# Optimization experiments

Measured on AMD Instinct MI355X. Metric: run time of the kernel, lower is better.

## Reference

```python
import jax, jax.numpy as jnp
import numpy as np

N_ATOMS = 500_000
N_BONDS = 600_000
N_MOL = 25_000
DEG_COUNTS = [100_000, 175_000, 150_000, 75_000]  # degrees 1..4, sum = N_ATOMS
ATOM_F, BOND_F = 62, 6
HID, FP = 100, 512


def setup_inputs() -> dict:
    key = jax.random.key(0)
    ks = jax.random.split(key, 32)
    inp = {}
    inp['atom_features'] = jax.random.normal(ks[0], (N_ATOMS, ATOM_F), dtype=jnp.float32)
    inp['bond_features'] = jax.random.normal(ks[1], (N_BONDS, BOND_F), dtype=jnp.float32)
    for i, (name_a, name_b, n) in enumerate(zip(['an1','an2','an3','an4'], ['bn1','bn2','bn3','bn4'], DEG_COUNTS)):
        d = i + 1
        inp[name_a] = jax.random.randint(ks[2 + 2*i], (n, d), 0, N_ATOMS, dtype=jnp.int32)
        inp[name_b] = jax.random.randint(ks[3 + 2*i], (n, d), 0, N_BONDS, dtype=jnp.int32)
    inp['mol_ids'] = jnp.repeat(jnp.arange(N_MOL, dtype=jnp.int32), N_ATOMS // N_MOL)
    dims = [(ATOM_F, HID), (HID, HID), (HID, FP)]
    for li, (din, dout) in enumerate(dims):
        inp[f'Wself{li}'] = jax.random.normal(ks[12 + li], (din, dout), dtype=jnp.float32) * (din ** -0.5)
        inp[f'bself{li}'] = jax.random.normal(ks[15 + li], (dout,), dtype=jnp.float32) * 0.01
        inp[f'Wd{li}'] = jax.random.normal(ks[18 + li], (4, din + BOND_F, dout), dtype=jnp.float32) * ((din + BOND_F) ** -0.5)
        inp[f'bd{li}'] = jax.random.normal(ks[21 + li], (4, dout), dtype=jnp.float32) * 0.01
    return inp


def _forward(atom_features, bond_features, ans, bns, mol_ids, self_params, deg_params):
    x = atom_features
    for (Ws, bs), (Wd, bd) in zip(self_params, deg_params):
        self_logits = x @ Ws + bs                      # [N, out]
        neigh = []
        for d in range(4):                             # degrees 1..4 (structurally distinct)
            a_sum = x[ans[d]].sum(axis=1)              # [n_d, F_in]  gather + reduce over degree
            b_sum = bond_features[bns[d]].sum(axis=1)  # [n_d, BOND_F]
            h = jnp.concatenate([a_sum, b_sum], axis=1)
            neigh.append(h @ Wd[d] + bd[d])
        neighbors_logits = jnp.concatenate(neigh, axis=0)  # atoms sorted by degree
        t = neighbors_logits + self_logits
        norm = jnp.linalg.norm(t, axis=1, keepdims=True)   # F.normalize (L2, eps=1e-12)
        x = jax.nn.relu(t / jnp.maximum(norm, 1e-12))
    return jax.ops.segment_sum(x, mol_ids, num_segments=N_MOL)  # sum_and_stack


def reference(atom_features, bond_features, an1, an2, an3, an4, bn1, bn2, bn3, bn4,
              mol_ids, Wself0, bself0, Wself1, bself1, Wself2, bself2,
              Wd0, bd0, Wd1, bd1, Wd2, bd2):
    ans = (an1, an2, an3, an4)
    bns = (bn1, bn2, bn3, bn4)
    self_params = ((Wself0, bself0), (Wself1, bself1), (Wself2, bself2))
    deg_params = ((Wd0, bd0), (Wd1, bd1), (Wd2, bd2))
    return _forward(atom_features, bond_features, ans, bns, mol_ids, self_params, deg_params)
```

## Files before the change

### kernel.cpp

```cpp
#include <hip/hip_runtime.h>


#define XS 100

typedef __attribute__((ext_vector_type(8))) short short8;
typedef __attribute__((ext_vector_type(4))) float float4v;

__device__ __forceinline__ float bf2f(unsigned u) { return __uint_as_float(u << 16); }
__device__ __forceinline__ unsigned short f2bf(float f) {
    unsigned b = __float_as_uint(f);
    return (unsigned short)((b + 0x7FFFu + ((b >> 16) & 1u)) >> 16);
}
__device__ __forceinline__ unsigned pack2(float a, float b) {
    return (unsigned)f2bf(a) | ((unsigned)f2bf(b) << 16);
}

__global__ void prep_weights(const float* __restrict__ Ws, const float* __restrict__ bs,
                             const float* __restrict__ Wd, const float* __restrict__ bd,
                             int F_IN, int F_OUT, int F_OUT_PAD, int KP, int SELF_PAD,
                             unsigned short* __restrict__ Wt, float* __restrict__ bc)
{
    int id = blockIdx.x * 256 + threadIdx.x;
    int total = 4 * F_OUT_PAD * KP;
    if (id >= total) return;
    int k  = id % KP;
    int nq = (id / KP) % F_OUT_PAD;
    int dg = id / (KP * F_OUT_PAD);
    float v = 0.f;
    if (nq < F_OUT) {
        if (k < F_IN)                                   v = Ws[(size_t)k * F_OUT + nq];
        else if (k >= SELF_PAD && k < SELF_PAD + F_IN)  v = Wd[((size_t)dg * (F_IN + 6) + (k - SELF_PAD)) * F_OUT + nq];
        else if (k >= 2 * SELF_PAD && k < 2 * SELF_PAD + 6)
            v = Wd[((size_t)dg * (F_IN + 6) + F_IN + (k - 2 * SELF_PAD)) * F_OUT + nq];
    }
    Wt[id] = f2bf(v);
    if (k == 0)
        bc[dg * F_OUT_PAD + nq] = (nq < F_OUT) ? (bs[nq] + bd[(size_t)dg * F_OUT + nq]) : 0.f;
}

template<int DEG, int SP>
__device__ __forceinline__ void gather_bf16(
    unsigned short* Hs, const unsigned short* __restrict__ x,
    const float* __restrict__ bondf,
    const int* __restrict__ an, const int* __restrict__ bn,
    int seg, int B40)
{
    const int tid = threadIdx.x;
    const int ch  = tid & 31;
    const int rr  = tid >> 5;

    if (ch < 25) {
        int ai[5][DEG];
        #pragma unroll
        for (int p = 0; p < 5; ++p) {
            const int ri = B40 + rr + 8 * p;
            #pragma unroll
            for (int d = 0; d < DEG; ++d) ai[p][d] = an[(size_t)ri * DEG + d];
        }
        uint2 sv[5], nv[5][DEG];
        #pragma unroll
        for (int p = 0; p < 5; ++p) {
            const int atom = seg + B40 + rr + 8 * p;
            sv[p] = *(const uint2*)(x + (size_t)atom * XS + ch * 4);
            #pragma unroll
            for (int d = 0; d < DEG; ++d)
                nv[p][d] = *(const uint2*)(x + (size_t)ai[p][d] * XS + ch * 4);
        }
        #pragma unroll
        for (int p = 0; p < 5; ++p) {
            unsigned short* hrow = Hs + (rr + 8 * p) * SP;
            *(uint2*)(hrow + ch * 4) = sv[p];
            float s0 = 0.f, s1 = 0.f, s2 = 0.f, s3 = 0.f;
            #pragma unroll
            for (int d = 0; d < DEG; ++d) {
                s0 += bf2f(nv[p][d].x & 0xFFFFu); s1 += bf2f(nv[p][d].x >> 16);
                s2 += bf2f(nv[p][d].y & 0xFFFFu); s3 += bf2f(nv[p][d].y >> 16);
            }
            uint2 o; o.x = pack2(s0, s1); o.y = pack2(s2, s3);
            *(uint2*)(hrow + 104 + ch * 4) = o;
        }
    }
    if (tid < 40) {
        const int ri = B40 + tid;
        int bi[DEG];
        #pragma unroll
        for (int d = 0; d < DEG; ++d) bi[d] = bn[(size_t)ri * DEG + d];
        float2 v0[DEG], v1[DEG], v2[DEG];
        #pragma unroll
        for (int d = 0; d < DEG; ++d) {
            const float* bp = bondf + (size_t)bi[d] * 6;
            v0[d] = *(const float2*)bp;
            v1[d] = *(const float2*)(bp + 2);
            v2[d] = *(const float2*)(bp + 4);
        }
        float s0 = 0.f, s1 = 0.f, s2 = 0.f, s3 = 0.f, s4 = 0.f, s5 = 0.f;
        #pragma unroll
        for (int d = 0; d < DEG; ++d) {
            s0 += v0[d].x; s1 += v0[d].y; s2 += v1[d].x;
            s3 += v1[d].y; s4 += v2[d].x; s5 += v2[d].y;
        }
        unsigned short* hrow = Hs + tid * SP;
        uint4 w; w.x = pack2(s0, s1); w.y = pack2(s2, s3); w.z = pack2(s4, s5); w.w = 0;
        *(uint4*)(hrow + 208) = w;
        *(uint4*)(hrow + 216) = make_uint4(0, 0, 0, 0);
    }
    for (int i = tid; i < 80; i += 256) {
        unsigned short* p = Hs + (i >> 1) * SP + ((i & 1) ? 204 : 100);
        *(uint2*)p = make_uint2(0, 0);
    }
    for (int i = tid; i < 8 * 28; i += 256) {
        *(uint4*)(Hs + (40 + i / 28) * SP + (i % 28) * 8) = make_uint4(0, 0, 0, 0);
    }
}

template<int DEG, int SP>
__device__ __forceinline__ void gather_f32(
    unsigned short* Hs, const float* __restrict__ x,
    const float* __restrict__ bondf,
    const int* __restrict__ an, const int* __restrict__ bn,
    int seg, int B40)
{
    const int tid = threadIdx.x;
    const int ch  = tid & 31;
    const int rr  = tid >> 5;

    if (ch < 31) {
        int ai[5][DEG];
        #pragma unroll
        for (int p = 0; p < 5; ++p) {
            const int ri = B40 + rr + 8 * p;
            #pragma unroll
            for (int d = 0; d < DEG; ++d) ai[p][d] = an[(size_t)ri * DEG + d];
        }
        float2 sv[5], nv[5][DEG];
        #pragma unroll
        for (int p = 0; p < 5; ++p) {
            const int atom = seg + B40 + rr + 8 * p;
            sv[p] = *(const float2*)(x + (size_t)atom * 62 + ch * 2);
            #pragma unroll
            for (int d = 0; d < DEG; ++d)
                nv[p][d] = *(const float2*)(x + (size_t)ai[p][d] * 62 + ch * 2);
        }
        #pragma unroll
        for (int p = 0; p < 5; ++p) {
            unsigned short* hrow = Hs + (rr + 8 * p) * SP;
            *(unsigned*)(hrow + ch * 2) = pack2(sv[p].x, sv[p].y);
            float s0 = 0.f, s1 = 0.f;
            #pragma unroll
            for (int d = 0; d < DEG; ++d) { s0 += nv[p][d].x; s1 += nv[p][d].y; }
            *(unsigned*)(hrow + 64 + ch * 2) = pack2(s0, s1);
        }
    }
    if (tid < 40) {
        const int ri = B40 + tid;
        int bi[DEG];
        #pragma unroll
        for (int d = 0; d < DEG; ++d) bi[d] = bn[(size_t)ri * DEG + d];
        float2 v0[DEG], v1[DEG], v2[DEG];
        #pragma unroll
        for (int d = 0; d < DEG; ++d) {
            const float* bp = bondf + (size_t)bi[d] * 6;
            v0[d] = *(const float2*)bp;
            v1[d] = *(const float2*)(bp + 2);
            v2[d] = *(const float2*)(bp + 4);
        }
        float s0 = 0.f, s1 = 0.f, s2 = 0.f, s3 = 0.f, s4 = 0.f, s5 = 0.f;
        #pragma unroll
        for (int d = 0; d < DEG; ++d) {
            s0 += v0[d].x; s1 += v0[d].y; s2 += v1[d].x;
            s3 += v1[d].y; s4 += v2[d].x; s5 += v2[d].y;
        }
        unsigned short* hrow = Hs + tid * SP;
        uint4 w; w.x = pack2(s0, s1); w.y = pack2(s2, s3); w.z = pack2(s4, s5); w.w = 0;
        *(uint4*)(hrow + 128) = w;
        *(uint4*)(hrow + 136) = make_uint4(0, 0, 0, 0);
        *(uint4*)(hrow + 144) = make_uint4(0, 0, 0, 0);
        *(uint4*)(hrow + 152) = make_uint4(0, 0, 0, 0);
    }
    for (int i = tid; i < 80; i += 256) {
        *(unsigned*)(Hs + (i >> 1) * SP + ((i & 1) ? 126 : 62)) = 0;
    }
    for (int i = tid; i < 8 * 20; i += 256) {
        *(uint4*)(Hs + (40 + i / 20) * SP + (i % 20) * 8) = make_uint4(0, 0, 0, 0);
    }
}

template<int F_IN, int F_OUT, int F_OUT_PAD, int SELF_PAD, bool LAST, bool BF16IN>
__global__ __launch_bounds__(256) void layer_mfma(
    const void* __restrict__ xin,
    const float* __restrict__ bondf,
    const int* __restrict__ an1, const int* __restrict__ bn1,
    const int* __restrict__ an2, const int* __restrict__ bn2,
    const int* __restrict__ an3, const int* __restrict__ bn3,
    const int* __restrict__ an4, const int* __restrict__ bn4,
    const unsigned short* __restrict__ Wt,
    const float* __restrict__ bcomb,
    unsigned short* __restrict__ xout,
    float* __restrict__ molout)
{
    constexpr int KP   = (2 * SELF_PAD + 6 + 31) & ~31;
    constexpr int SP   = KP + 8;
    constexpr int NT   = F_OUT_PAD / 16;
    constexpr int JMAX = (NT + 3) / 4;

    __shared__ __align__(16) unsigned short Hs[48 * SP];
    __shared__ float ssqs[4][48];

    const int R0 = blockIdx.x * 40;
    int deg, seg;
    if (R0 < 100000)      { deg = 1; seg = 0;      }
    else if (R0 < 275000) { deg = 2; seg = 100000; }
    else if (R0 < 425000) { deg = 3; seg = 275000; }
    else                  { deg = 4; seg = 425000; }
    const int B40 = R0 - seg;

    if constexpr (BF16IN) {
        const unsigned short* x = (const unsigned short*)xin;
        switch (deg) {
            case 1: gather_bf16<1, SP>(Hs, x, bondf, an1, bn1, seg, B40); break;
            case 2: gather_bf16<2, SP>(Hs, x, bondf, an2, bn2, seg, B40); break;
            case 3: gather_bf16<3, SP>(Hs, x, bondf, an3, bn3, seg, B40); break;
            default: gather_bf16<4, SP>(Hs, x, bondf, an4, bn4, seg, B40); break;
        }
    } else {
        const float* x = (const float*)xin;
        switch (deg) {
            case 1: gather_f32<1, SP>(Hs, x, bondf, an1, bn1, seg, B40); break;
            case 2: gather_f32<2, SP>(Hs, x, bondf, an2, bn2, seg, B40); break;
            case 3: gather_f32<3, SP>(Hs, x, bondf, an3, bn3, seg, B40); break;
            default: gather_f32<4, SP>(Hs, x, bondf, an4, bn4, seg, B40); break;
        }
    }
    __syncthreads();

    const int lane = threadIdx.x & 63;
    const int wv   = threadIdx.x >> 6;
    const int n16  = lane & 15;
    const int quad = lane >> 4;

    float4v acc[JMAX][3];
    #pragma unroll
    for (int j = 0; j < JMAX; ++j)
        #pragma unroll
        for (int mt = 0; mt < 3; ++mt)
            acc[j][mt] = (float4v){0.f, 0.f, 0.f, 0.f};

    const unsigned short* Wb = Wt + (size_t)(deg - 1) * F_OUT_PAD * KP;

    for (int kk = 0; kk < KP; kk += 32) {
        short8 a[3];
        #pragma unroll
        for (int mt = 0; mt < 3; ++mt)
            a[mt] = *(const short8*)&Hs[(mt * 16 + n16) * SP + kk + quad * 8];
        short8 b[JMAX];
        #pragma unroll
        for (int j = 0; j < JMAX; ++j) {
            const int nt = wv + 4 * j;
            if (nt < NT)
                b[j] = *(const short8*)(Wb + (size_t)(nt * 16 + n16) * KP + kk + quad * 8);
        }
        #pragma unroll
        for (int j = 0; j < JMAX; ++j) {
            const int nt = wv + 4 * j;
            if (nt < NT)
                #pragma unroll
                for (int mt = 0; mt < 3; ++mt)
                    acc[j][mt] = __builtin_amdgcn_mfma_f32_16x16x32_bf16(
                        a[mt], b[j], acc[j][mt], 0, 0, 0);
        }
    }

    float ssq[3][4];
    #pragma unroll
    for (int mt = 0; mt < 3; ++mt)
        #pragma unroll
        for (int r = 0; r < 4; ++r) ssq[mt][r] = 0.f;

    #pragma unroll
    for (int j = 0; j < JMAX; ++j) {
        const int nt = wv + 4 * j;
        if (nt < NT) {
            const float bj = bcomb[(deg - 1) * F_OUT_PAD + nt * 16 + n16];
            #pragma unroll
            for (int mt = 0; mt < 3; ++mt)
                #pragma unroll
                for (int r = 0; r < 4; ++r) {
                    float t = acc[j][mt][r] + bj;
                    acc[j][mt][r] = t;
                    ssq[mt][r] += t * t;
                }
        }
    }
    #pragma unroll
    for (int off = 1; off <= 8; off <<= 1)
        #pragma unroll
        for (int mt = 0; mt < 3; ++mt)
            #pragma unroll
            for (int r = 0; r < 4; ++r)
                ssq[mt][r] += __shfl_xor(ssq[mt][r], off);
    if (n16 == 0)
        #pragma unroll
        for (int mt = 0; mt < 3; ++mt)
            #pragma unroll
            for (int r = 0; r < 4; ++r)
                ssqs[wv][mt * 16 + quad * 4 + r] = ssq[mt][r];
    __syncthreads();

    float rn[3][4];
    #pragma unroll
    for (int mt = 0; mt < 3; ++mt)
        #pragma unroll
        for (int r = 0; r < 4; ++r) {
            const int row = mt * 16 + quad * 4 + r;
            const float s = ssqs[0][row] + ssqs[1][row] + ssqs[2][row] + ssqs[3][row];
            rn[mt][r] = 1.0f / fmaxf(sqrtf(s), 1e-12f);
        }

    if constexpr (!LAST) {
        #pragma unroll
        for (int j = 0; j < JMAX; ++j) {
            const int nt = wv + 4 * j;
            if (nt < NT) {
                const int col = nt * 16 + n16;
                if (col < F_OUT) {
                    #pragma unroll
                    for (int mt = 0; mt < 3; ++mt)
                        #pragma unroll
                        for (int r = 0; r < 4; ++r) {
                            const int row = mt * 16 + quad * 4 + r;
                            if (row < 40) {
                                const float v = fmaxf(acc[j][mt][r] * rn[mt][r], 0.f);
                                xout[(size_t)(R0 + row) * XS + col] = f2bf(v);
                            }
                        }
                }
            }
        }
    } else {
        #pragma unroll
        for (int j = 0; j < JMAX; ++j) {
            float m0 = 0.f, m1 = 0.f;
            #pragma unroll
            for (int mt = 0; mt < 3; ++mt)
                #pragma unroll
                for (int r = 0; r < 4; ++r) {
                    const int row = mt * 16 + quad * 4 + r;
                    if (row < 40) {
                        const float v = fmaxf(acc[j][mt][r] * rn[mt][r], 0.f);
                        if (row < 20) m0 += v; else m1 += v;
                    }
                }
            m0 += __shfl_xor(m0, 16); m0 += __shfl_xor(m0, 32);
            m1 += __shfl_xor(m1, 16); m1 += __shfl_xor(m1, 32);
            if (quad == 0) {
                const int col = (wv + 4 * j) * 16 + n16;
                molout[(size_t)(2 * blockIdx.x)     * 512 + col] = m0;
                molout[(size_t)(2 * blockIdx.x + 1) * 512 + col] = m1;
            }
        }
    }
}

extern "C" void kernel_launch(void* const* d_in, const int* in_sizes, int n_in,
                              void* d_out, int out_size, void* d_ws, size_t ws_size,
                              hipStream_t stream) {
    const bool sig_order = (in_sizes[3] != 100000);

    const float* atomf = (const float*)d_in[0];
    const float* bondf = (const float*)d_in[1];
    const int *an1, *bn1, *an2, *bn2, *an3, *bn3, *an4, *bn4;
    const float *Ws0, *bs0, *Wd0, *bd0;
    const float *Ws1, *bs1, *Wd1, *bd1;
    const float *Ws2, *bs2, *Wd2, *bd2;

    if (!sig_order) {
        an1 = (const int*)d_in[2];  bn1 = (const int*)d_in[3];
        an2 = (const int*)d_in[4];  bn2 = (const int*)d_in[5];
        an3 = (const int*)d_in[6];  bn3 = (const int*)d_in[7];
        an4 = (const int*)d_in[8];  bn4 = (const int*)d_in[9];
        Ws0 = (const float*)d_in[11]; bs0 = (const float*)d_in[12];
        Wd0 = (const float*)d_in[13]; bd0 = (const float*)d_in[14];
        Ws1 = (const float*)d_in[15]; bs1 = (const float*)d_in[16];
        Wd1 = (const float*)d_in[17]; bd1 = (const float*)d_in[18];
        Ws2 = (const float*)d_in[19]; bs2 = (const float*)d_in[20];
        Wd2 = (const float*)d_in[21]; bd2 = (const float*)d_in[22];
    } else {
        an1 = (const int*)d_in[2];  an2 = (const int*)d_in[3];
        an3 = (const int*)d_in[4];  an4 = (const int*)d_in[5];
        bn1 = (const int*)d_in[6];  bn2 = (const int*)d_in[7];
        bn3 = (const int*)d_in[8];  bn4 = (const int*)d_in[9];
        Ws0 = (const float*)d_in[11]; bs0 = (const float*)d_in[12];
        Ws1 = (const float*)d_in[13]; bs1 = (const float*)d_in[14];
        Ws2 = (const float*)d_in[15]; bs2 = (const float*)d_in[16];
        Wd0 = (const float*)d_in[17]; bd0 = (const float*)d_in[18];
        Wd1 = (const float*)d_in[19]; bd1 = (const float*)d_in[20];
        Wd2 = (const float*)d_in[21]; bd2 = (const float*)d_in[22];
    }

    char* w = (char*)d_ws;
    unsigned short* x1  = (unsigned short*)w;
    unsigned short* x2  = (unsigned short*)(w + 100000000);
    unsigned short* Wt0 = (unsigned short*)(w + 200000000);
    float*          bc0 = (float*)(w + 200143360);
    unsigned short* Wt1 = (unsigned short*)(w + 200145152);
    float*          bc1 = (float*)(w + 200345856);
    unsigned short* Wt2 = (unsigned short*)(w + 200347648);
    float*          bc2 = (float*)(w + 201265152);

    prep_weights<<<(4 * 112 * 160 + 255) / 256, 256, 0, stream>>>(
        Ws0, bs0, Wd0, bd0, 62, 100, 112, 160, 64, Wt0, bc0);
    prep_weights<<<(4 * 112 * 224 + 255) / 256, 256, 0, stream>>>(
        Ws1, bs1, Wd1, bd1, 100, 100, 112, 224, 104, Wt1, bc1);
    prep_weights<<<(4 * 512 * 224 + 255) / 256, 256, 0, stream>>>(
        Ws2, bs2, Wd2, bd2, 100, 512, 512, 224, 104, Wt2, bc2);

    dim3 grid(12500), block(256);
    layer_mfma<62, 100, 112, 64, false, false><<<grid, block, 0, stream>>>(
        atomf, bondf, an1, bn1, an2, bn2, an3, bn3, an4, bn4,
        Wt0, bc0, x1, nullptr);
    layer_mfma<100, 100, 112, 104, false, true><<<grid, block, 0, stream>>>(
        x1, bondf, an1, bn1, an2, bn2, an3, bn3, an4, bn4,
        Wt1, bc1, x2, nullptr);
    layer_mfma<100, 512, 512, 104, true, true><<<grid, block, 0, stream>>>(
        x2, bondf, an1, bn1, an2, bn2, an3, bn3, an4, bn4,
        Wt2, bc2, nullptr, (float*)d_out);
}
```

Before: 899.5 us.

## Double block size to 512 threads and spread gather and MFMA work over eight waves

```diff
diff --git a/kernel.cpp b/kernel.cpp
--- a/kernel.cpp
+++ b/kernel.cpp
@@ -47,70 +47,79 @@
 {
     const int tid = threadIdx.x;
     const int ch  = tid & 31;
-    const int rr  = tid >> 5;
+    const int rg  = tid >> 5;
 
     if (ch < 25) {
-        int ai[5][DEG];
-        #pragma unroll
-        for (int p = 0; p < 5; ++p) {
-            const int ri = B40 + rr + 8 * p;
-            #pragma unroll
-            for (int d = 0; d < DEG; ++d) ai[p][d] = an[(size_t)ri * DEG + d];
-        }
-        uint2 sv[5], nv[5][DEG];
-        #pragma unroll
-        for (int p = 0; p < 5; ++p) {
-            const int atom = seg + B40 + rr + 8 * p;
-            sv[p] = *(const uint2*)(x + (size_t)atom * XS + ch * 4);
-            #pragma unroll
-            for (int d = 0; d < DEG; ++d)
-                nv[p][d] = *(const uint2*)(x + (size_t)ai[p][d] * XS + ch * 4);
-        }
-        #pragma unroll
-        for (int p = 0; p < 5; ++p) {
-            unsigned short* hrow = Hs + (rr + 8 * p) * SP;
-            *(uint2*)(hrow + ch * 4) = sv[p];
-            float s0 = 0.f, s1 = 0.f, s2 = 0.f, s3 = 0.f;
+        int ai[3][DEG];
+        #pragma unroll
+        for (int p = 0; p < 3; ++p) {
+            const int r = rg + 16 * p;
+            if (r < 40) {
+                const int ri = B40 + r;
+                #pragma unroll
+                for (int d = 0; d < DEG; ++d) ai[p][d] = an[(size_t)ri * DEG + d];
+            }
+        }
+        uint2 sv[3], nv[3][DEG];
+        #pragma unroll
+        for (int p = 0; p < 3; ++p) {
+            const int r = rg + 16 * p;
+            if (r < 40) {
+                sv[p] = *(const uint2*)(x + (size_t)(seg + B40 + r) * XS + ch * 4);
+                #pragma unroll
+                for (int d = 0; d < DEG; ++d)
+                    nv[p][d] = *(const uint2*)(x + (size_t)ai[p][d] * XS + ch * 4);
+            }
+        }
+        #pragma unroll
+        for (int p = 0; p < 3; ++p) {
+            const int r = rg + 16 * p;
+            if (r < 40) {
+                unsigned short* hrow = Hs + r * SP;
+                *(uint2*)(hrow + ch * 4) = sv[p];
+                float s0 = 0.f, s1 = 0.f, s2 = 0.f, s3 = 0.f;
+                #pragma unroll
+                for (int d = 0; d < DEG; ++d) {
+                    s0 += bf2f(nv[p][d].x & 0xFFFFu); s1 += bf2f(nv[p][d].x >> 16);
+                    s2 += bf2f(nv[p][d].y & 0xFFFFu); s3 += bf2f(nv[p][d].y >> 16);
+                }
+                uint2 o; o.x = pack2(s0, s1); o.y = pack2(s2, s3);
+                *(uint2*)(hrow + 104 + ch * 4) = o;
+            }
+        }
+    } else {
+        const int idx = rg * 7 + (ch - 25);
+        if (idx < 40) {
+            const int ri = B40 + idx;
+            int bi[DEG];
+            #pragma unroll
+            for (int d = 0; d < DEG; ++d) bi[d] = bn[(size_t)ri * DEG + d];
+            float2 v0[DEG], v1[DEG], v2[DEG];
             #pragma unroll
             for (int d = 0; d < DEG; ++d) {
-                s0 += bf2f(nv[p][d].x & 0xFFFFu); s1 += bf2f(nv[p][d].x >> 16);
-                s2 += bf2f(nv[p][d].y & 0xFFFFu); s3 += bf2f(nv[p][d].y >> 16);
-            }
-            uint2 o; o.x = pack2(s0, s1); o.y = pack2(s2, s3);
-            *(uint2*)(hrow + 104 + ch * 4) = o;
-        }
-    }
-    if (tid < 40) {
-        const int ri = B40 + tid;
-        int bi[DEG];
-        #pragma unroll
-        for (int d = 0; d < DEG; ++d) bi[d] = bn[(size_t)ri * DEG + d];
-        float2 v0[DEG], v1[DEG], v2[DEG];
-        #pragma unroll
-        for (int d = 0; d < DEG; ++d) {
-            const float* bp = bondf + (size_t)bi[d] * 6;
-            v0[d] = *(const float2*)bp;
-            v1[d] = *(const float2*)(bp + 2);
-            v2[d] = *(const float2*)(bp + 4);
-        }
-        float s0 = 0.f, s1 = 0.f, s2 = 0.f, s3 = 0.f, s4 = 0.f, s5 = 0.f;
-        #pragma unroll
-        for (int d = 0; d < DEG; ++d) {
-            s0 += v0[d].x; s1 += v0[d].y; s2 += v1[d].x;
-            s3 += v1[d].y; s4 += v2[d].x; s5 += v2[d].y;
-        }
-        unsigned short* hrow = Hs + tid * SP;
-        uint4 w; w.x = pack2(s0, s1); w.y = pack2(s2, s3); w.z = pack2(s4, s5); w.w = 0;
-        *(uint4*)(hrow + 208) = w;
-        *(uint4*)(hrow + 216) = make_uint4(0, 0, 0, 0);
-    }
-    for (int i = tid; i < 80; i += 256) {
+                const float* bp = bondf + (size_t)bi[d] * 6;
+                v0[d] = *(const float2*)bp;
+                v1[d] = *(const float2*)(bp + 2);
+                v2[d] = *(const float2*)(bp + 4);
+            }
+            float s0 = 0.f, s1 = 0.f, s2 = 0.f, s3 = 0.f, s4 = 0.f, s5 = 0.f;
+            #pragma unroll
+            for (int d = 0; d < DEG; ++d) {
+                s0 += v0[d].x; s1 += v0[d].y; s2 += v1[d].x;
+                s3 += v1[d].y; s4 += v2[d].x; s5 += v2[d].y;
+            }
+            unsigned short* hrow = Hs + idx * SP;
+            uint4 w; w.x = pack2(s0, s1); w.y = pack2(s2, s3); w.z = pack2(s4, s5); w.w = 0;
+            *(uint4*)(hrow + 208) = w;
+            *(uint4*)(hrow + 216) = make_uint4(0, 0, 0, 0);
+        }
+    }
+    for (int i = tid; i < 80; i += 512) {
         unsigned short* p = Hs + (i >> 1) * SP + ((i & 1) ? 204 : 100);
         *(uint2*)p = make_uint2(0, 0);
     }
-    for (int i = tid; i < 8 * 28; i += 256) {
+    for (int i = tid; i < 8 * 28; i += 512)
         *(uint4*)(Hs + (40 + i / 28) * SP + (i % 28) * 8) = make_uint4(0, 0, 0, 0);
-    }
 }
 
 template<int DEG, int SP>
@@ -122,33 +131,41 @@
 {
     const int tid = threadIdx.x;
     const int ch  = tid & 31;
-    const int rr  = tid >> 5;
+    const int rg  = tid >> 5;
 
     if (ch < 31) {
-        int ai[5][DEG];
-        #pragma unroll
-        for (int p = 0; p < 5; ++p) {
-            const int ri = B40 + rr + 8 * p;
-            #pragma unroll
-            for (int d = 0; d < DEG; ++d) ai[p][d] = an[(size_t)ri * DEG + d];
-        }
-        float2 sv[5], nv[5][DEG];
-        #pragma unroll
-        for (int p = 0; p < 5; ++p) {
-            const int atom = seg + B40 + rr + 8 * p;
-            sv[p] = *(const float2*)(x + (size_t)atom * 62 + ch * 2);
-            #pragma unroll
-            for (int d = 0; d < DEG; ++d)
-                nv[p][d] = *(const float2*)(x + (size_t)ai[p][d] * 62 + ch * 2);
-        }
-        #pragma unroll
-        for (int p = 0; p < 5; ++p) {
-            unsigned short* hrow = Hs + (rr + 8 * p) * SP;
-            *(unsigned*)(hrow + ch * 2) = pack2(sv[p].x, sv[p].y);
-            float s0 = 0.f, s1 = 0.f;
-            #pragma unroll
-            for (int d = 0; d < DEG; ++d) { s0 += nv[p][d].x; s1 += nv[p][d].y; }
-            *(unsigned*)(hrow + 64 + ch * 2) = pack2(s0, s1);
+        int ai[3][DEG];
+        #pragma unroll
+        for (int p = 0; p < 3; ++p) {
+            const int r = rg + 16 * p;
+            if (r < 40) {
+                const int ri = B40 + r;
+                #pragma unroll
+                for (int d = 0; d < DEG; ++d) ai[p][d] = an[(size_t)ri * DEG + d];
+            }
+        }
+        float2 sv[3], nv[3][DEG];
+        #pragma unroll
+        for (int p = 0; p < 3; ++p) {
+            const int r = rg + 16 * p;
+            if (r < 40) {
+                sv[p] = *(const float2*)(x + (size_t)(seg + B40 + r) * 62 + ch * 2);
+                #pragma unroll
+                for (int d = 0; d < DEG; ++d)
+                    nv[p][d] = *(const float2*)(x + (size_t)ai[p][d] * 62 + ch * 2);
+            }
+        }
+        #pragma unroll
+        for (int p = 0; p < 3; ++p) {
+            const int r = rg + 16 * p;
+            if (r < 40) {
+                unsigned short* hrow = Hs + r * SP;
+                *(unsigned*)(hrow + ch * 2) = pack2(sv[p].x, sv[p].y);
+                float s0 = 0.f, s1 = 0.f;
+                #pragma unroll
+                for (int d = 0; d < DEG; ++d) { s0 += nv[p][d].x; s1 += nv[p][d].y; }
+                *(unsigned*)(hrow + 64 + ch * 2) = pack2(s0, s1);
+            }
         }
     }
     if (tid < 40) {
@@ -177,16 +194,14 @@
         *(uint4*)(hrow + 144) = make_uint4(0, 0, 0, 0);
         *(uint4*)(hrow + 152) = make_uint4(0, 0, 0, 0);
     }
-    for (int i = tid; i < 80; i += 256) {
+    for (int i = tid; i < 80; i += 512)
         *(unsigned*)(Hs + (i >> 1) * SP + ((i & 1) ? 126 : 62)) = 0;
-    }
-    for (int i = tid; i < 8 * 20; i += 256) {
+    for (int i = tid; i < 8 * 20; i += 512)
         *(uint4*)(Hs + (40 + i / 20) * SP + (i % 20) * 8) = make_uint4(0, 0, 0, 0);
-    }
 }
 
 template<int F_IN, int F_OUT, int F_OUT_PAD, int SELF_PAD, bool LAST, bool BF16IN>
-__global__ __launch_bounds__(256) void layer_mfma(
+__global__ __launch_bounds__(512, 4) void layer_mfma(
     const void* __restrict__ xin,
     const float* __restrict__ bondf,
     const int* __restrict__ an1, const int* __restrict__ bn1,
@@ -201,10 +216,10 @@
     constexpr int KP   = (2 * SELF_PAD + 6 + 31) & ~31;
     constexpr int SP   = KP + 8;
     constexpr int NT   = F_OUT_PAD / 16;
-    constexpr int JMAX = (NT + 3) / 4;
+    constexpr int JMAX = (NT + 7) / 8;
 
     __shared__ __align__(16) unsigned short Hs[48 * SP];
-    __shared__ float ssqs[4][48];
+    __shared__ float ssqs[8][48];
 
     const int R0 = blockIdx.x * 40;
     int deg, seg;
@@ -255,13 +270,13 @@
         short8 b[JMAX];
         #pragma unroll
         for (int j = 0; j < JMAX; ++j) {
-            const int nt = wv + 4 * j;
+            const int nt = wv + 8 * j;
             if (nt < NT)
                 b[j] = *(const short8*)(Wb + (size_t)(nt * 16 + n16) * KP + kk + quad * 8);
         }
         #pragma unroll
         for (int j = 0; j < JMAX; ++j) {
-            const int nt = wv + 4 * j;
+            const int nt = wv + 8 * j;
             if (nt < NT)
                 #pragma unroll
                 for (int mt = 0; mt < 3; ++mt)
@@ -278,7 +293,7 @@
 
     #pragma unroll
     for (int j = 0; j < JMAX; ++j) {
-        const int nt = wv + 4 * j;
+        const int nt = wv + 8 * j;
         if (nt < NT) {
             const float bj = bcomb[(deg - 1) * F_OUT_PAD + nt * 16 + n16];
             #pragma unroll
@@ -312,14 +327,16 @@
         #pragma unroll
         for (int r = 0; r < 4; ++r) {
             const int row = mt * 16 + quad * 4 + r;
-            const float s = ssqs[0][row] + ssqs[1][row] + ssqs[2][row] + ssqs[3][row];
+            float s = 0.f;
+            #pragma unroll
+            for (int w = 0; w < 8; ++w) s += ssqs[w][row];
             rn[mt][r] = 1.0f / fmaxf(sqrtf(s), 1e-12f);
         }
 
     if constexpr (!LAST) {
         #pragma unroll
         for (int j = 0; j < JMAX; ++j) {
-            const int nt = wv + 4 * j;
+            const int nt = wv + 8 * j;
             if (nt < NT) {
                 const int col = nt * 16 + n16;
                 if (col < F_OUT) {
@@ -353,7 +370,7 @@
             m0 += __shfl_xor(m0, 16); m0 += __shfl_xor(m0, 32);
             m1 += __shfl_xor(m1, 16); m1 += __shfl_xor(m1, 32);
             if (quad == 0) {
-                const int col = (wv + 4 * j) * 16 + n16;
+                const int col = (wv + 8 * j) * 16 + n16;
                 molout[(size_t)(2 * blockIdx.x)     * 512 + col] = m0;
                 molout[(size_t)(2 * blockIdx.x + 1) * 512 + col] = m1;
             }
@@ -414,7 +431,7 @@
     prep_weights<<<(4 * 512 * 224 + 255) / 256, 256, 0, stream>>>(
         Ws2, bs2, Wd2, bd2, 100, 512, 512, 224, 104, Wt2, bc2);
 
-    dim3 grid(12500), block(256);
+    dim3 grid(12500), block(512);
     layer_mfma<62, 100, 112, 64, false, false><<<grid, block, 0, stream>>>(
         atomf, bondf, an1, bn1, an2, bn2, an3, bn3, an4, bn4,
         Wt0, bc0, x1, nullptr);
```

Result: slower. 969.2 us (+7.8%).

## Use 512-thread blocks for final layer with matching gather and norm reduction

Applied to the files above, without the earlier changes.

```diff
diff --git a/kernel.cpp b/kernel.cpp
--- a/kernel.cpp
+++ b/kernel.cpp
@@ -13,6 +13,12 @@
 }
 __device__ __forceinline__ unsigned pack2(float a, float b) {
     return (unsigned)f2bf(a) | ((unsigned)f2bf(b) << 16);
+}
+__device__ __forceinline__ void rowseg(int r, int& deg, int& seg) {
+    if (r < 100000)      { deg = 1; seg = 0;      }
+    else if (r < 275000) { deg = 2; seg = 100000; }
+    else if (r < 425000) { deg = 3; seg = 275000; }
+    else                 { deg = 4; seg = 425000; }
 }
 
 __global__ void prep_weights(const float* __restrict__ Ws, const float* __restrict__ bs,
@@ -39,7 +45,7 @@
 }
 
 template<int DEG, int SP>
-__device__ __forceinline__ void gather_bf16(
+__device__ __forceinline__ void g256_bf16(
     unsigned short* Hs, const unsigned short* __restrict__ x,
     const float* __restrict__ bondf,
     const int* __restrict__ an, const int* __restrict__ bn,
@@ -48,7 +54,6 @@
     const int tid = threadIdx.x;
     const int ch  = tid & 31;
     const int rr  = tid >> 5;
-
     if (ch < 25) {
         int ai[5][DEG];
         #pragma unroll
@@ -108,13 +113,12 @@
         unsigned short* p = Hs + (i >> 1) * SP + ((i & 1) ? 204 : 100);
         *(uint2*)p = make_uint2(0, 0);
     }
-    for (int i = tid; i < 8 * 28; i += 256) {
+    for (int i = tid; i < 8 * 28; i += 256)
         *(uint4*)(Hs + (40 + i / 28) * SP + (i % 28) * 8) = make_uint4(0, 0, 0, 0);
-    }
 }
 
 template<int DEG, int SP>
-__device__ __forceinline__ void gather_f32(
+__device__ __forceinline__ void g256_f32(
     unsigned short* Hs, const float* __restrict__ x,
     const float* __restrict__ bondf,
     const int* __restrict__ an, const int* __restrict__ bn,
@@ -123,7 +127,6 @@
     const int tid = threadIdx.x;
     const int ch  = tid & 31;
     const int rr  = tid >> 5;
-
     if (ch < 31) {
         int ai[5][DEG];
         #pragma unroll
@@ -177,16 +180,97 @@
         *(uint4*)(hrow + 144) = make_uint4(0, 0, 0, 0);
         *(uint4*)(hrow + 152) = make_uint4(0, 0, 0, 0);
     }
-    for (int i = tid; i < 80; i += 256) {
+    for (int i = tid; i < 80; i += 256)
         *(unsigned*)(Hs + (i >> 1) * SP + ((i & 1) ? 126 : 62)) = 0;
-    }
-    for (int i = tid; i < 8 * 20; i += 256) {
+    for (int i = tid; i < 8 * 20; i += 256)
         *(uint4*)(Hs + (40 + i / 20) * SP + (i % 20) * 8) = make_uint4(0, 0, 0, 0);
-    }
-}
-
-template<int F_IN, int F_OUT, int F_OUT_PAD, int SELF_PAD, bool LAST, bool BF16IN>
-__global__ __launch_bounds__(256) void layer_mfma(
+}
+
+template<int DEG, int SP>
+__device__ __forceinline__ void g512_bf16(
+    unsigned short* Hs, const unsigned short* __restrict__ x,
+    const float* __restrict__ bondf,
+    const int* __restrict__ an, const int* __restrict__ bn,
+    int seg, int B40)
+{
+    const int tid = threadIdx.x;
+    const int ch  = tid & 31;
+    const int rg  = tid >> 5;
+    if (ch < 25) {
+        int ai[3][DEG];
+        #pragma unroll
+        for (int p = 0; p < 3; ++p) {
+            const int r = rg + 16 * p;
+            if (r < 40) {
+                const int ri = B40 + r;
+                #pragma unroll
+                for (int d = 0; d < DEG; ++d) ai[p][d] = an[(size_t)ri * DEG + d];
+            }
+        }
+        uint2 sv[3], nv[3][DEG];
+        #pragma unroll
+        for (int p = 0; p < 3; ++p) {
+            const int r = rg + 16 * p;
+            if (r < 40) {
+                sv[p] = *(const uint2*)(x + (size_t)(seg + B40 + r) * XS + ch * 4);
+                #pragma unroll
+                for (int d = 0; d < DEG; ++d)
+                    nv[p][d] = *(const uint2*)(x + (size_t)ai[p][d] * XS + ch * 4);
+            }
+        }
+        #pragma unroll
+        for (int p = 0; p < 3; ++p) {
+            const int r = rg + 16 * p;
+            if (r < 40) {
+                unsigned short* hrow = Hs + r * SP;
+                *(uint2*)(hrow + ch * 4) = sv[p];
+                float s0 = 0.f, s1 = 0.f, s2 = 0.f, s3 = 0.f;
+                #pragma unroll
+                for (int d = 0; d < DEG; ++d) {
+                    s0 += bf2f(nv[p][d].x & 0xFFFFu); s1 += bf2f(nv[p][d].x >> 16);
+                    s2 += bf2f(nv[p][d].y & 0xFFFFu); s3 += bf2f(nv[p][d].y >> 16);
+                }
+                uint2 o; o.x = pack2(s0, s1); o.y = pack2(s2, s3);
+                *(uint2*)(hrow + 104 + ch * 4) = o;
+            }
+        }
+    } else {
+        const int idx = rg * 7 + (ch - 25);
+        if (idx < 40) {
+            const int ri = B40 + idx;
+            int bi[DEG];
+            #pragma unroll
+            for (int d = 0; d < DEG; ++d) bi[d] = bn[(size_t)ri * DEG + d];
+            float2 v0[DEG], v1[DEG], v2[DEG];
+            #pragma unroll
+            for (int d = 0; d < DEG; ++d) {
+                const float* bp = bondf + (size_t)bi[d] * 6;
+                v0[d] = *(const float2*)bp;
+                v1[d] = *(const float2*)(bp + 2);
+                v2[d] = *(const float2*)(bp + 4);
+            }
+            float s0 = 0.f, s1 = 0.f, s2 = 0.f, s3 = 0.f, s4 = 0.f, s5 = 0.f;
+            #pragma unroll
+            for (int d = 0; d < DEG; ++d) {
+                s0 += v0[d].x; s1 += v0[d].y; s2 += v1[d].x;
+                s3 += v1[d].y; s4 += v2[d].x; s5 += v2[d].y;
+            }
+            unsigned short* hrow = Hs + idx * SP;
+            uint4 w; w.x = pack2(s0, s1); w.y = pack2(s2, s3); w.z = pack2(s4, s5); w.w = 0;
+            *(uint4*)(hrow + 208) = w;
+            *(uint4*)(hrow + 216) = make_uint4(0, 0, 0, 0);
+        }
+    }
+    for (int i = tid; i < 80; i += 512) {
+        unsigned short* p = Hs + (i >> 1) * SP + ((i & 1) ? 204 : 100);
+        *(uint2*)p = make_uint2(0, 0);
+    }
+    for (int i = tid; i < 8 * 28; i += 512)
+        *(uint4*)(Hs + (40 + i / 28) * SP + (i % 28) * 8) = make_uint4(0, 0, 0, 0);
+}
+
+template<int F_IN, int F_OUT, int F_OUT_PAD, int SELF_PAD, bool LAST, bool BF16IN, int BLK>
+__global__ __launch_bounds__(BLK, BLK == 512 ? 4 : 2) void layer_fused(
     const void* __restrict__ xin,
     const float* __restrict__ bondf,
     const int* __restrict__ an1, const int* __restrict__ bn1,
@@ -201,34 +285,41 @@
     constexpr int KP   = (2 * SELF_PAD + 6 + 31) & ~31;
     constexpr int SP   = KP + 8;
     constexpr int NT   = F_OUT_PAD / 16;
-    constexpr int JMAX = (NT + 3) / 4;
+    constexpr int NW   = BLK / 64;
+    constexpr int JMAX = (NT + NW - 1) / NW;
 
     __shared__ __align__(16) unsigned short Hs[48 * SP];
-    __shared__ float ssqs[4][48];
+    __shared__ float ssqs[NW][48];
+    __shared__ __align__(16) float rn48[48];
 
     const int R0 = blockIdx.x * 40;
-    int deg, seg;
-    if (R0 < 100000)      { deg = 1; seg = 0;      }
-    else if (R0 < 275000) { deg = 2; seg = 100000; }
-    else if (R0 < 425000) { deg = 3; seg = 275000; }
-    else                  { deg = 4; seg = 425000; }
+    int deg, seg; rowseg(R0, deg, seg);
     const int B40 = R0 - seg;
 
     if constexpr (BF16IN) {
         const unsigned short* x = (const unsigned short*)xin;
-        switch (deg) {
-            case 1: gather_bf16<1, SP>(Hs, x, bondf, an1, bn1, seg, B40); break;
-            case 2: gather_bf16<2, SP>(Hs, x, bondf, an2, bn2, seg, B40); break;
-            case 3: gather_bf16<3, SP>(Hs, x, bondf, an3, bn3, seg, B40); break;
-            default: gather_bf16<4, SP>(Hs, x, bondf, an4, bn4, seg, B40); break;
+        if constexpr (BLK == 256) {
+            switch (deg) {
+                case 1: g256_bf16<1, SP>(Hs, x, bondf, an1, bn1, seg, B40); break;
+                case 2: g256_bf16<2, SP>(Hs, x, bondf, an2, bn2, seg, B40); break;
+                case 3: g256_bf16<3, SP>(Hs, x, bondf, an3, bn3, seg, B40); break;
+                default: g256_bf16<4, SP>(Hs, x, bondf, an4, bn4, seg, B40); break;
+            }
+        } else {
+            switch (deg) {
+                case 1: g512_bf16<1, SP>(Hs, x, bondf, an1, bn1, seg, B40); break;
+                case 2: g512_bf16<2, SP>(Hs, x, bondf, an2, bn2, seg, B40); break;
+                case 3: g512_bf16<3, SP>(Hs, x, bondf, an3, bn3, seg, B40); break;
+                default: g512_bf16<4, SP>(Hs, x, bondf, an4, bn4, seg, B40); break;
+            }
         }
     } else {
         const float* x = (const float*)xin;
         switch (deg) {
-            case 1: gather_f32<1, SP>(Hs, x, bondf, an1, bn1, seg, B40); break;
-            case 2: gather_f32<2, SP>(Hs, x, bondf, an2, bn2, seg, B40); break;
-            case 3: gather_f32<3, SP>(Hs, x, bondf, an3, bn3, seg, B40); break;
-            default: gather_f32<4, SP>(Hs, x, bondf, an4, bn4, seg, B40); break;
+            case 1: g256_f32<1, SP>(Hs, x, bondf, an1, bn1, seg, B40); break;
+            case 2: g256_f32<2, SP>(Hs, x, bondf, an2, bn2, seg, B40); break;
+            case 3: g256_f32<3, SP>(Hs, x, bondf, an3, bn3, seg, B40); break;
+            default: g256_f32<4, SP>(Hs, x, bondf, an4, bn4, seg, B40); break;
         }
     }
     __syncthreads();
@@ -247,6 +338,7 @@
 
     const unsigned short* Wb = Wt + (size_t)(deg - 1) * F_OUT_PAD * KP;
 
+    #pragma unroll
     for (int kk = 0; kk < KP; kk += 32) {
         short8 a[3];
         #pragma unroll
@@ -255,13 +347,13 @@
         short8 b[JMAX];
         #pragma unroll
         for (int j = 0; j < JMAX; ++j) {
-            const int nt = wv + 4 * j;
+            const int nt = wv + NW * j;
             if (nt < NT)
                 b[j] = *(const short8*)(Wb + (size_t)(nt * 16 + n16) * KP + kk + quad * 8);
         }
         #pragma unroll
         for (int j = 0; j < JMAX; ++j) {
-            const int nt = wv + 4 * j;
+            const int nt = wv + NW * j;
             if (nt < NT)
                 #pragma unroll
                 for (int mt = 0; mt < 3; ++mt)
@@ -278,7 +370,7 @@
 
     #pragma unroll
     for (int j = 0; j < JMAX; ++j) {
-        const int nt = wv + 4 * j;
+        const int nt = wv + NW * j;
         if (nt < NT) {
             const float bj = bcomb[(deg - 1) * F_OUT_PAD + nt * 16 + n16];
             #pragma unroll
@@ -306,20 +398,25 @@
                 ssqs[wv][mt * 16 + quad * 4 + r] = ssq[mt][r];
     __syncthreads();
 
+    if (threadIdx.x < 48) {
+        float s = 0.f;
+        #pragma unroll
+        for (int w = 0; w < NW; ++w) s += ssqs[w][threadIdx.x];
+        rn48[threadIdx.x] = 1.0f / fmaxf(sqrtf(s), 1e-12f);
+    }
+    __syncthreads();
+
     float rn[3][4];
     #pragma unroll
-    for (int mt = 0; mt < 3; ++mt)
-        #pragma unroll
-        for (int r = 0; r < 4; ++r) {
-            const int row = mt * 16 + quad * 4 + r;
-            const float s = ssqs[0][row] + ssqs[1][row] + ssqs[2][row] + ssqs[3][row];
-            rn[mt][r] = 1.0f / fmaxf(sqrtf(s), 1e-12f);
-        }
+    for (int mt = 0; mt < 3; ++mt) {
+        float4 v = *(const float4*)&rn48[mt * 16 + quad * 4];
+        rn[mt][0] = v.x; rn[mt][1] = v.y; rn[mt][2] = v.z; rn[mt][3] = v.w;
+    }
 
     if constexpr (!LAST) {
         #pragma unroll
         for (int j = 0; j < JMAX; ++j) {
-            const int nt = wv + 4 * j;
+            const int nt = wv + NW * j;
             if (nt < NT) {
                 const int col = nt * 16 + n16;
                 if (col < F_OUT) {
@@ -353,7 +450,7 @@
             m0 += __shfl_xor(m0, 16); m0 += __shfl_xor(m0, 32);
             m1 += __shfl_xor(m1, 16); m1 += __shfl_xor(m1, 32);
             if (quad == 0) {
-                const int col = (wv + 4 * j) * 16 + n16;
+                const int col = (wv + NW * j) * 16 + n16;
                 molout[(size_t)(2 * blockIdx.x)     * 512 + col] = m0;
                 molout[(size_t)(2 * blockIdx.x + 1) * 512 + col] = m1;
             }
@@ -414,14 +511,13 @@
     prep_weights<<<(4 * 512 * 224 + 255) / 256, 256, 0, stream>>>(
         Ws2, bs2, Wd2, bd2, 100, 512, 512, 224, 104, Wt2, bc2);
 
-    dim3 grid(12500), block(256);
-    layer_mfma<62, 100, 112, 64, false, false><<<grid, block, 0, stream>>>(
+    layer_fused<62, 100, 112, 64, false, false, 256><<<12500, 256, 0, stream>>>(
         atomf, bondf, an1, bn1, an2, bn2, an3, bn3, an4, bn4,
         Wt0, bc0, x1, nullptr);
-    layer_mfma<100, 100, 112, 104, false, true><<<grid, block, 0, stream>>>(
+    layer_fused<100, 100, 112, 104, false, true, 256><<<12500, 256, 0, stream>>>(
         x1, bondf, an1, bn1, an2, bn2, an3, bn3, an4, bn4,
         Wt1, bc1, x2, nullptr);
-    layer_mfma<100, 512, 512, 104, true, true><<<grid, block, 0, stream>>>(
+    layer_fused<100, 512, 512, 104, true, true, 512><<<12500, 512, 0, stream>>>(
         x2, bondf, an1, bn1, an2, bn2, an3, bn3, an4, bn4,
         Wt2, bc2, nullptr, (float*)d_out);
 }
```

Result: faster. 826.4 us (-8.1%).
